# Optimization experiments

Measured on AMD Instinct MI355X. Metric: run time of the kernel, lower is better.

## Reference

```python
import jax, jax.numpy as jnp
import numpy as np

B, S, D = 4, 1024, 1024
E, F, TOPK = 16, 512, 4


def setup_inputs() -> dict:
    key = jax.random.key(0)
    k1, k2, k3, k4, k5 = jax.random.split(key, 5)
    scale = 0.02
    return {
        "x": jax.random.normal(k1, (B, S, D), dtype=jnp.float32),
        "Wr": jax.random.normal(k2, (D, E), dtype=jnp.float32) * scale,   # router
        "Wg": jax.random.normal(k3, (E, D, F), dtype=jnp.float32) * scale,  # gate proj
        "Wu": jax.random.normal(k4, (E, D, F), dtype=jnp.float32) * scale,  # up proj
        "Wd": jax.random.normal(k5, (E, F, D), dtype=jnp.float32) * scale,  # down proj
    }


def reference(x, Wr, Wg, Wu, Wd):
    b, s, d = x.shape
    xf = x.reshape(-1, d)                      # [N, D], N = B*S
    n = xf.shape[0]
    e = Wr.shape[1]

    # --- router: softmax over experts, top-k, renormalized weights ---
    probs = jax.nn.softmax(xf @ Wr, axis=-1)   # [N, E]
    w, idx = jax.lax.top_k(probs, TOPK)        # [N, K], [N, K]
    w = w / jnp.sum(w, axis=-1, keepdims=True)

    # combine weights per (token, expert); zero for unselected experts.
    # Equivalent to the per-expert where/gather/scatter-add loop in torch.
    cw = jnp.zeros((n, e), dtype=xf.dtype).at[jnp.arange(n)[:, None], idx].add(w)

    # --- per-expert gated FFN (SwiGLU), combined with routing weights ---
    def body(acc, ws):
        wg, wu, wd, c = ws                     # [D,F], [D,F], [F,D], [N]
        h = jax.nn.silu(xf @ wg) * (xf @ wu)   # [N, F]
        return acc + c[:, None] * (h @ wd), None

    out, _ = jax.lax.scan(body, jnp.zeros_like(xf), (Wg, Wu, Wd, cw.T))
    return out.reshape(b, s, d)
```

## Files before the change

### kernel.cpp

```cpp
#include <hip/hip_runtime.h>

#define N_TOK 4096
#define DIM   1024
#define NE    16
#define NF    512
#define TOPK  4
#define CAP   4096
#define NPAIR (N_TOK * TOPK)
#define MAXTILES 144
#define GU_BLOCKS (8 * MAXTILES)
#define PREPD_BLOCKS (NE * 128)

typedef _Float16 v8h __attribute__((ext_vector_type(8)));
typedef float    v4f __attribute__((ext_vector_type(4)));

__device__ __forceinline__ void prep_tile(
    const float* __restrict__ src, unsigned short* __restrict__ dst,
    int R, int C, int RIL, int e, int cbl, int rbl, float (*tile)[65])
{
    int c0 = cbl * 64, r0 = rbl * 64;
    const float* s = src + (size_t)e * R * C;
    int t = threadIdx.x;
    int tr = t >> 4, tc = (t & 15) * 4;
#pragma unroll
    for (int i = 0; i < 4; i++) {
        int row = i * 16 + tr;
        float4 v = *(const float4*)(s + (size_t)(r0 + row) * C + c0 + tc);
        tile[row][tc + 0] = v.x; tile[row][tc + 1] = v.y;
        tile[row][tc + 2] = v.z; tile[row][tc + 3] = v.w;
    }
    __syncthreads();
    int ktPerE = R >> 5;
    int cbPerE = C >> RIL;
    int imgSz  = (1 << RIL) * 32;
#pragma unroll
    for (int i = 0; i < 4; i++) {
        int nr = i * 16 + tr;
        int orow = c0 + nr;
        int k0 = r0 + tc;
        int cb = orow >> RIL;
        int r  = orow & ((1 << RIL) - 1);
        int kt = k0 >> 5;
        size_t off = ((size_t)(e * cbPerE + cb) * ktPerE + kt) * imgSz
                   + r * 32 + (k0 & 31);
        union { unsigned short u[4]; uint2 v; } p;
#pragma unroll
        for (int j = 0; j < 4; j++)
            p.u[j] = __builtin_bit_cast(unsigned short, (_Float16)tile[tc + j][nr]);
        *(uint2*)(dst + off) = p.v;
    }
}

__global__ __launch_bounds__(256) void router_prep_kernel(
    const float* __restrict__ x, const float* __restrict__ Wr,
    const float* __restrict__ Wg, const float* __restrict__ Wu,
    int* __restrict__ tokIdx, float* __restrict__ tokW,
    unsigned short* __restrict__ xb,
    unsigned short* __restrict__ Wg_t, unsigned short* __restrict__ Wu_t)
{
    __shared__ __align__(16) float tile[64][65];
    int bid = blockIdx.x;
    if (bid >= 1024) {
        int pid = bid - 1024;
        int z = pid >> 7;
        int which = z >> 4, e = z & 15;
        int bx = pid & 127;
        int cbl = bx & 7, rbl = bx >> 3;
        prep_tile(which ? Wu : Wg, which ? Wu_t : Wg_t,
                  DIM, NF, 6, e, cbl, rbl, tile);
        return;
    }
    int tid = threadIdx.x;
    int w = tid >> 6, l = tid & 63;
    int t = bid * 4 + w;

    double z[NE];
#pragma unroll
    for (int e = 0; e < NE; e++) z[e] = 0.0;
    const float* xrow = x + (size_t)t * DIM;
#pragma unroll
    for (int i = 0; i < 16; i++) {
        int d = i * 64 + l;
        double xv = (double)xrow[d];
        const float4* wr = (const float4*)(Wr + d * NE);
        float4 w0 = wr[0], w1 = wr[1], w2 = wr[2], w3 = wr[3];
        z[0]  += xv * w0.x; z[1]  += xv * w0.y; z[2]  += xv * w0.z; z[3]  += xv * w0.w;
        z[4]  += xv * w1.x; z[5]  += xv * w1.y; z[6]  += xv * w1.z; z[7]  += xv * w1.w;
        z[8]  += xv * w2.x; z[9]  += xv * w2.y; z[10] += xv * w2.z; z[11] += xv * w2.w;
        z[12] += xv * w3.x; z[13] += xv * w3.y; z[14] += xv * w3.z; z[15] += xv * w3.w;
    }
    const float4* xv4 = (const float4*)xrow;
#pragma unroll
    for (int h2 = 0; h2 < 2; h2++) {
        int base = h2 * 512 + l * 8;
        float4 a = xv4[h2 * 128 + l * 2];
        float4 b = xv4[h2 * 128 + l * 2 + 1];
        union { unsigned short u[8]; uint4 v; } p;
        p.u[0] = __builtin_bit_cast(unsigned short, (_Float16)a.x);
        p.u[1] = __builtin_bit_cast(unsigned short, (_Float16)a.y);
        p.u[2] = __builtin_bit_cast(unsigned short, (_Float16)a.z);
        p.u[3] = __builtin_bit_cast(unsigned short, (_Float16)a.w);
        p.u[4] = __builtin_bit_cast(unsigned short, (_Float16)b.x);
        p.u[5] = __builtin_bit_cast(unsigned short, (_Float16)b.y);
        p.u[6] = __builtin_bit_cast(unsigned short, (_Float16)b.z);
        p.u[7] = __builtin_bit_cast(unsigned short, (_Float16)b.w);
        *(uint4*)(xb + (size_t)t * DIM + base) = p.v;
    }
#pragma unroll
    for (int e = 0; e < NE; e++) {
#pragma unroll
        for (int m = 1; m < 64; m <<= 1) z[e] += __shfl_xor(z[e], m, 64);
    }
    if (l == 0) {
        bool taken[NE];
#pragma unroll
        for (int e = 0; e < NE; e++) taken[e] = false;
        int idx[TOPK]; double sel[TOPK];
        for (int k = 0; k < TOPK; k++) {
            int bi = 0; double bv = -1.0e300;
            for (int e = 0; e < NE; e++)
                if (!taken[e] && z[e] > bv) { bv = z[e]; bi = e; }
            taken[bi] = true; idx[k] = bi; sel[k] = bv;
        }
        double m = sel[0];
        double ex[TOPK]; double s = 0.0;
        for (int k = 0; k < TOPK; k++) { ex[k] = exp(sel[k] - m); s += ex[k]; }
        for (int k = 0; k < TOPK; k++) {
            tokIdx[t * TOPK + k] = idx[k];
            tokW[t * TOPK + k]   = (float)(ex[k] / s);
        }
    }
}

__global__ __launch_bounds__(256) void bin_kernel(
    const int* __restrict__ tokIdx,
    int* __restrict__ cnt, int* __restrict__ bpair)
{
    int e = blockIdx.x;
    int tid = threadIdx.x, lane = tid & 63, wv = tid >> 6;
    __shared__ int wsum[4];
    __shared__ int sbase;
    if (tid == 0) sbase = 0;
    __syncthreads();
    unsigned long long lt = (1ULL << lane) - 1ULL;
#pragma unroll 1
    for (int c0 = 0; c0 < NPAIR; c0 += 1024) {
        int i0 = c0 + tid * 4;
        int4 v = *(const int4*)(tokIdx + i0);
        int m[4] = {v.x == e, v.y == e, v.z == e, v.w == e};
        int r[4]; int wcnt = 0;
#pragma unroll
        for (int j = 0; j < 4; j++) {
            unsigned long long bal = __ballot(m[j] != 0);
            r[j] = wcnt + __popcll(bal & lt);
            wcnt += __popcll(bal);
        }
        if (lane == 0) wsum[wv] = wcnt;
        __syncthreads();
        int woff = sbase;
        for (int k = 0; k < wv; k++) woff += wsum[k];
#pragma unroll
        for (int j = 0; j < 4; j++)
            if (m[j]) bpair[e * CAP + woff + r[j]] = i0 + j;
        __syncthreads();
        if (tid == 0) sbase += wsum[0] + wsum[1] + wsum[2] + wsum[3];
        __syncthreads();
    }
    if (tid == 0) cnt[e] = sbase;
}

__device__ __forceinline__ int ldsw(int row, int chunk) {
    return row * 32 + (chunk ^ ((row >> 1) & 3)) * 8;
}

__device__ __forceinline__ void gload16(const unsigned short* g, unsigned short* l) {
    __builtin_amdgcn_global_load_lds(
        (const __attribute__((address_space(1))) void*)g,
        (__attribute__((address_space(3))) void*)l, 16, 0, 0);
}

__device__ __forceinline__ bool find_tile(const int* __restrict__ cnt,
                                          int ti, int& e, int& mt, int& tbase) {
    int rt = 0;
#pragma unroll 1
    for (int ee = 0; ee < NE; ee++) {
        int nt = (cnt[ee] + 127) >> 7;
        if (ti < rt + nt) { e = ee; mt = ti - rt; tbase = rt; return true; }
        rt += nt;
    }
    return false;
}

__global__ __launch_bounds__(256) void ffn_gate_up_kernel(
    const unsigned short* __restrict__ xb,
    const unsigned short* __restrict__ Wg_t,
    const unsigned short* __restrict__ Wu_t,
    const int* __restrict__ cnt,
    const int* __restrict__ bpair,
    unsigned short* __restrict__ h_t,
    const float* __restrict__ Wd,
    unsigned short* __restrict__ Wd_t)
{
    __shared__ __align__(16) unsigned char smem[33536];
    unsigned short* sX = (unsigned short*)smem;
    unsigned short* sG = (unsigned short*)(smem + 16384);
    unsigned short* sU = (unsigned short*)(smem + 24576);
    int* sTok = (int*)(smem + 32768);
    float (*tile)[65] = (float (*)[65])smem;

    int bid = blockIdx.x;
    if (bid >= GU_BLOCKS) {
        int pid = bid - GU_BLOCKS;
        int e = pid >> 7;
        int bx = pid & 127;
        int cbl = bx & 15, rbl = bx >> 4;
        prep_tile(Wd, Wd_t, NF, DIM, 7, e, cbl, rbl, tile);
        return;
    }
    int fb = bid & 7, ti = bid >> 3;
    int e, mt, tbase;
    if (!find_tile(cnt, ti, e, mt, tbase)) return;
    int count = cnt[e];

    int tid = threadIdx.x, lane = tid & 63, w = tid >> 6;
    if (tid < 128) {
        int pos = mt * 128 + tid;
        sTok[tid] = bpair[e * CAP + min(pos, count - 1)] >> 2;
    }
    __syncthreads();

    int srow0 = w * 16 + (lane >> 2);
    int srow1 = srow0 + 64;
    int spos  = lane & 3;
    int cx0 = spos ^ ((srow0 >> 1) & 3);
    int cx1 = spos ^ ((srow1 >> 1) & 3);
    const unsigned short* gX0 = xb + (size_t)sTok[srow0] * DIM + cx0 * 8;
    const unsigned short* gX1 = xb + (size_t)sTok[srow1] * DIM + cx1 * 8;
    const unsigned short* gG  = Wg_t + ((size_t)(e * 8 + fb) * 32) * 2048 + srow0 * 32 + cx0 * 8;
    const unsigned short* gU  = Wu_t + ((size_t)(e * 8 + fb) * 32) * 2048 + srow0 * 32 + cx0 * 8;
    unsigned short* dX0 = sX + (size_t)(w * 16) * 32;
    unsigned short* dX1 = sX + (size_t)(64 + w * 16) * 32;
    unsigned short* dG  = sG + (size_t)(w * 16) * 32;
    unsigned short* dU  = sU + (size_t)(w * 16) * 32;

    int row = lane & 15, q = lane >> 4;
    int rw = w & 1, cw = w >> 1;
    int aoff[4], goff[2];
#pragma unroll
    for (int mi = 0; mi < 4; mi++) aoff[mi] = ldsw(rw * 64 + mi * 16 + row, q);
#pragma unroll
    for (int ni = 0; ni < 2; ni++) goff[ni] = ldsw(cw * 32 + ni * 16 + row, q);

    v4f accG[4][2], accU[4][2];
    v4f zero = {0.f, 0.f, 0.f, 0.f};
#pragma unroll
    for (int mi = 0; mi < 4; mi++)
#pragma unroll
        for (int ni = 0; ni < 2; ni++) { accG[mi][ni] = zero; accU[mi][ni] = zero; }

#define STAGE_GU(b, kt) do {                                   \
        gload16(gX0 + (kt) * 32, dX0 + (b) * 4096);            \
        gload16(gX1 + (kt) * 32, dX1 + (b) * 4096);            \
        gload16(gG + (size_t)(kt) * 2048, dG + (b) * 2048);    \
        gload16(gU + (size_t)(kt) * 2048, dU + (b) * 2048);    \
    } while (0)

    STAGE_GU(0, 0);
    __syncthreads();

#pragma unroll 1
    for (int kt = 0; kt < 32; kt++) {
        int buf = kt & 1;
        if (kt < 31) STAGE_GU(buf ^ 1, kt + 1);
        const unsigned short* bX = sX + buf * 4096;
        const unsigned short* bGp = sG + buf * 2048;
        const unsigned short* bUp = sU + buf * 2048;
        v8h a[4], bg[2], bu[2];
#pragma unroll
        for (int mi = 0; mi < 4; mi++) a[mi] = *(const v8h*)&bX[aoff[mi]];
#pragma unroll
        for (int ni = 0; ni < 2; ni++) {
            bg[ni] = *(const v8h*)&bGp[goff[ni]];
            bu[ni] = *(const v8h*)&bUp[goff[ni]];
        }
#pragma unroll
        for (int mi = 0; mi < 4; mi++)
#pragma unroll
            for (int ni = 0; ni < 2; ni++) {
                accG[mi][ni] = __builtin_amdgcn_mfma_f32_16x16x32_f16(a[mi], bg[ni], accG[mi][ni], 0, 0, 0);
                accU[mi][ni] = __builtin_amdgcn_mfma_f32_16x16x32_f16(a[mi], bu[ni], accU[mi][ni], 0, 0, 0);
            }
        __syncthreads();
    }
#undef STAGE_GU

    size_t himg = (size_t)(tbase + mt) * 16;
#pragma unroll
    for (int mi = 0; mi < 4; mi++)
#pragma unroll
        for (int ni = 0; ni < 2; ni++) {
            int f = fb * 64 + cw * 32 + ni * 16 + row;
#pragma unroll
            for (int i = 0; i < 4; i++) {
                int rl = rw * 64 + mi * 16 + q * 4 + i;
                int pos = mt * 128 + rl;
                if (pos < count) {
                    float gv = accG[mi][ni][i];
                    float uv = accU[mi][ni][i];
                    float hv = gv * uv / (1.0f + __expf(-gv));
                    size_t off = (himg + (f >> 5)) * 4096 + rl * 32 + (f & 31);
                    h_t[off] = __builtin_bit_cast(unsigned short, (_Float16)hv);
                }
            }
        }
}

__global__ __launch_bounds__(256) void ffn_down_kernel(
    const unsigned short* __restrict__ h_t,
    const unsigned short* __restrict__ Wd_t,
    const int* __restrict__ cnt,
    const int* __restrict__ bpair,
    unsigned short* __restrict__ part)
{
    int ti = blockIdx.x, db = blockIdx.y;
    int e, mt, tbase;
    if (!find_tile(cnt, ti, e, mt, tbase)) return;
    int count = cnt[e];

    __shared__ __align__(16) unsigned short sH[2 * 128 * 32];
    __shared__ __align__(16) unsigned short sW[2 * 128 * 32];
    __shared__ int sPair[128];

    int tid = threadIdx.x, lane = tid & 63, w = tid >> 6;
    if (tid < 128) {
        int pos = mt * 128 + tid;
        sPair[tid] = bpair[e * CAP + min(pos, count - 1)];
    }
    __syncthreads();

    int srow0 = w * 16 + (lane >> 2);
    int srow1 = srow0 + 64;
    int spos  = lane & 3;
    int c0 = spos ^ ((srow0 >> 1) & 3);
    int c1 = spos ^ ((srow1 >> 1) & 3);
    const unsigned short* hbase = h_t + ((size_t)(tbase + mt) * 16) * 4096;
    const unsigned short* wbase = Wd_t + ((size_t)(e * 8 + db) * 16) * 4096;
    const unsigned short* gH0 = hbase + srow0 * 32 + c0 * 8;
    const unsigned short* gH1 = hbase + srow1 * 32 + c1 * 8;
    const unsigned short* gW0 = wbase + srow0 * 32 + c0 * 8;
    const unsigned short* gW1 = wbase + srow1 * 32 + c1 * 8;
    unsigned short* dH0 = sH + (size_t)(w * 16) * 32;
    unsigned short* dH1 = sH + (size_t)(64 + w * 16) * 32;
    unsigned short* dW0 = sW + (size_t)(w * 16) * 32;
    unsigned short* dW1 = sW + (size_t)(64 + w * 16) * 32;

    int row = lane & 15, q = lane >> 4;
    int rw = w & 1, cw = w >> 1;
    int aoff[4], boff[4];
#pragma unroll
    for (int mi = 0; mi < 4; mi++) aoff[mi] = ldsw(rw * 64 + mi * 16 + row, q);
#pragma unroll
    for (int ni = 0; ni < 4; ni++) boff[ni] = ldsw(cw * 64 + ni * 16 + row, q);

    v4f acc[4][4];
    v4f zero = {0.f, 0.f, 0.f, 0.f};
#pragma unroll
    for (int mi = 0; mi < 4; mi++)
#pragma unroll
        for (int ni = 0; ni < 4; ni++) acc[mi][ni] = zero;

#define STAGE_D(b, kt) do {                                         \
        gload16(gH0 + (size_t)(kt) * 4096, dH0 + (b) * 4096);       \
        gload16(gH1 + (size_t)(kt) * 4096, dH1 + (b) * 4096);       \
        gload16(gW0 + (size_t)(kt) * 4096, dW0 + (b) * 4096);       \
        gload16(gW1 + (size_t)(kt) * 4096, dW1 + (b) * 4096);       \
    } while (0)

    STAGE_D(0, 0);
    __syncthreads();

#pragma unroll 1
    for (int kt = 0; kt < 16; kt++) {
        int buf = kt & 1;
        if (kt < 15) STAGE_D(buf ^ 1, kt + 1);
        const unsigned short* bH = sH + buf * 4096;
        const unsigned short* bW = sW + buf * 4096;
        v8h a[4], b[4];
#pragma unroll
        for (int mi = 0; mi < 4; mi++) a[mi] = *(const v8h*)&bH[aoff[mi]];
#pragma unroll
        for (int ni = 0; ni < 4; ni++) b[ni] = *(const v8h*)&bW[boff[ni]];
#pragma unroll
        for (int mi = 0; mi < 4; mi++)
#pragma unroll
            for (int ni = 0; ni < 4; ni++)
                acc[mi][ni] = __builtin_amdgcn_mfma_f32_16x16x32_f16(a[mi], b[ni], acc[mi][ni], 0, 0, 0);
        __syncthreads();
    }
#undef STAGE_D

#pragma unroll
    for (int mi = 0; mi < 4; mi++)
#pragma unroll
        for (int ni = 0; ni < 4; ni++) {
            int col = db * 128 + cw * 64 + ni * 16 + row;
#pragma unroll
            for (int i = 0; i < 4; i++) {
                int rl = rw * 64 + mi * 16 + q * 4 + i;
                int pos = mt * 128 + rl;
                if (pos < count) {
                    int p = sPair[rl];
                    part[(size_t)p * DIM + col] =
                        __builtin_bit_cast(unsigned short, (_Float16)acc[mi][ni][i]);
                }
            }
        }
}

__global__ __launch_bounds__(256) void combine_kernel(
    const unsigned short* __restrict__ part, const float* __restrict__ tokW,
    float* __restrict__ out)
{
    int gid = blockIdx.x * 256 + threadIdx.x;
    int t = gid >> 8;
    int c = (gid & 255) * 4;
    float4 r = {0.f, 0.f, 0.f, 0.f};
#pragma unroll
    for (int k = 0; k < TOPK; k++) {
        float wk = tokW[t * TOPK + k];
        union { uint2 u; _Float16 h[4]; } cv;
        cv.u = *(const uint2*)(part + ((size_t)(t * TOPK + k)) * DIM + c);
        r.x += wk * (float)cv.h[0];
        r.y += wk * (float)cv.h[1];
        r.z += wk * (float)cv.h[2];
        r.w += wk * (float)cv.h[3];
    }
    *(float4*)(out + (size_t)t * DIM + c) = r;
}

extern "C" void kernel_launch(void* const* d_in, const int* in_sizes, int n_in,
                              void* d_out, int out_size, void* d_ws, size_t ws_size,
                              hipStream_t stream)
{
    const float* x  = (const float*)d_in[0];
    const float* Wr = (const float*)d_in[1];
    const float* Wg = (const float*)d_in[2];
    const float* Wu = (const float*)d_in[3];
    const float* Wd = (const float*)d_in[4];
    float* out = (float*)d_out;
    char* ws = (char*)d_ws;

    size_t off = 0;
    int* tokIdx = (int*)(ws + off);   off += (size_t)NPAIR * 4;
    float* tokW = (float*)(ws + off); off += (size_t)NPAIR * 4;
    int* cnt    = (int*)(ws + off);   off += 256;
    int* bpair  = (int*)(ws + off);   off += (size_t)NE * CAP * 4;
    unsigned short* xb   = (unsigned short*)(ws + off); off += (size_t)N_TOK * DIM * 2;
    unsigned short* Wg_t = (unsigned short*)(ws + off); off += (size_t)NE * DIM * NF * 2;
    unsigned short* Wu_t = (unsigned short*)(ws + off); off += (size_t)NE * DIM * NF * 2;
    unsigned short* Wd_t = (unsigned short*)(ws + off); off += (size_t)NE * DIM * NF * 2;
    unsigned short* h_t  = (unsigned short*)(ws + off); off += (size_t)MAXTILES * 16 * 4096 * 2;
    unsigned short* part = (unsigned short*)(ws + off); off += (size_t)NPAIR * DIM * 2;

    router_prep_kernel<<<1024 + 4096, 256, 0, stream>>>(
        x, Wr, Wg, Wu, tokIdx, tokW, xb, Wg_t, Wu_t);
    bin_kernel<<<NE, 256, 0, stream>>>(tokIdx, cnt, bpair);
    ffn_gate_up_kernel<<<GU_BLOCKS + PREPD_BLOCKS, 256, 0, stream>>>(
        xb, Wg_t, Wu_t, cnt, bpair, h_t, Wd, Wd_t);
    ffn_down_kernel<<<dim3(MAXTILES, 8), 256, 0, stream>>>(
        h_t, Wd_t, cnt, bpair, part);
    combine_kernel<<<(N_TOK * DIM) / (256 * 4), 256, 0, stream>>>(part, tokW, out);
}
```

Before: 271.4 us.

## Fuse combine into down-proj via atomics and relax GEMM loop barriers

Removes the separate combine kernel and the fp16 partial buffer. The down-projection now scales each result by its routing weight and atomically adds it into the output, which is zeroed by extra blocks in the router kernel. Separately, both GEMM main loops replace __syncthreads with explicit vmcnt waits and raw s_barrier so the next stage's global loads stay in flight while the current tile is consumed. The cost is fp32 atomic contention (four adds per output element) and a nondeterministic summation order.

Result: slower. 300.2 us (+10.6%).

```diff
diff --git a/kernel.cpp b/kernel.cpp
--- a/kernel.cpp
+++ b/kernel.cpp
@@ -10,6 +10,9 @@
 #define MAXTILES 144
 #define GU_BLOCKS (8 * MAXTILES)
 #define PREPD_BLOCKS (NE * 128)
+#define RP_ROUTER 1024
+#define RP_PREP   4096
+#define RP_ZERO   256
 
 typedef _Float16 v8h __attribute__((ext_vector_type(8)));
 typedef float    v4f __attribute__((ext_vector_type(4)));
@@ -56,12 +59,21 @@
     const float* __restrict__ Wg, const float* __restrict__ Wu,
     int* __restrict__ tokIdx, float* __restrict__ tokW,
     unsigned short* __restrict__ xb,
-    unsigned short* __restrict__ Wg_t, unsigned short* __restrict__ Wu_t)
+    unsigned short* __restrict__ Wg_t, unsigned short* __restrict__ Wu_t,
+    float* __restrict__ out)
 {
     __shared__ __align__(16) float tile[64][65];
     int bid = blockIdx.x;
-    if (bid >= 1024) {
-        int pid = bid - 1024;
+    if (bid >= RP_ROUTER + RP_PREP) {
+        int zb = bid - (RP_ROUTER + RP_PREP);
+        float4 z4 = {0.f, 0.f, 0.f, 0.f};
+        float4* o4 = (float4*)out + (size_t)zb * 4096 + threadIdx.x;
+#pragma unroll
+        for (int i = 0; i < 16; i++) o4[i * 256] = z4;
+        return;
+    }
+    if (bid >= RP_ROUTER) {
+        int pid = bid - RP_ROUTER;
         int z = pid >> 7;
         int which = z >> 4, e = z & 15;
         int bx = pid & 127;
@@ -266,12 +278,18 @@
     } while (0)
 
     STAGE_GU(0, 0);
-    __syncthreads();
 
 #pragma unroll 1
     for (int kt = 0; kt < 32; kt++) {
         int buf = kt & 1;
-        if (kt < 31) STAGE_GU(buf ^ 1, kt + 1);
+        if (kt < 31) {
+            STAGE_GU(buf ^ 1, kt + 1);
+            asm volatile("s_waitcnt vmcnt(4)" ::: "memory");
+        } else {
+            asm volatile("s_waitcnt vmcnt(0)" ::: "memory");
+        }
+        __builtin_amdgcn_s_barrier();
+        __builtin_amdgcn_sched_barrier(0);
         const unsigned short* bX = sX + buf * 4096;
         const unsigned short* bGp = sG + buf * 2048;
         const unsigned short* bUp = sU + buf * 2048;
@@ -290,7 +308,9 @@
                 accG[mi][ni] = __builtin_amdgcn_mfma_f32_16x16x32_f16(a[mi], bg[ni], accG[mi][ni], 0, 0, 0);
                 accU[mi][ni] = __builtin_amdgcn_mfma_f32_16x16x32_f16(a[mi], bu[ni], accU[mi][ni], 0, 0, 0);
             }
-        __syncthreads();
+        __builtin_amdgcn_sched_barrier(0);
+        __builtin_amdgcn_s_barrier();
+        __builtin_amdgcn_sched_barrier(0);
     }
 #undef STAGE_GU
 
@@ -320,7 +340,8 @@
     const unsigned short* __restrict__ Wd_t,
     const int* __restrict__ cnt,
     const int* __restrict__ bpair,
-    unsigned short* __restrict__ part)
+    const float* __restrict__ tokW,
+    float* __restrict__ out)
 {
     int ti = blockIdx.x, db = blockIdx.y;
     int e, mt, tbase;
@@ -377,12 +398,18 @@
     } while (0)
 
     STAGE_D(0, 0);
-    __syncthreads();
 
 #pragma unroll 1
     for (int kt = 0; kt < 16; kt++) {
         int buf = kt & 1;
-        if (kt < 15) STAGE_D(buf ^ 1, kt + 1);
+        if (kt < 15) {
+            STAGE_D(buf ^ 1, kt + 1);
+            asm volatile("s_waitcnt vmcnt(4)" ::: "memory");
+        } else {
+            asm volatile("s_waitcnt vmcnt(0)" ::: "memory");
+        }
+        __builtin_amdgcn_s_barrier();
+        __builtin_amdgcn_sched_barrier(0);
         const unsigned short* bH = sH + buf * 4096;
         const unsigned short* bW = sW + buf * 4096;
         v8h a[4], b[4];
@@ -395,47 +422,29 @@
 #pragma unroll
             for (int ni = 0; ni < 4; ni++)
                 acc[mi][ni] = __builtin_amdgcn_mfma_f32_16x16x32_f16(a[mi], b[ni], acc[mi][ni], 0, 0, 0);
-        __syncthreads();
+        __builtin_amdgcn_sched_barrier(0);
+        __builtin_amdgcn_s_barrier();
+        __builtin_amdgcn_sched_barrier(0);
     }
 #undef STAGE_D
 
 #pragma unroll
     for (int mi = 0; mi < 4; mi++)
 #pragma unroll
-        for (int ni = 0; ni < 4; ni++) {
-            int col = db * 128 + cw * 64 + ni * 16 + row;
-#pragma unroll
-            for (int i = 0; i < 4; i++) {
-                int rl = rw * 64 + mi * 16 + q * 4 + i;
-                int pos = mt * 128 + rl;
-                if (pos < count) {
-                    int p = sPair[rl];
-                    part[(size_t)p * DIM + col] =
-                        __builtin_bit_cast(unsigned short, (_Float16)acc[mi][ni][i]);
+        for (int i = 0; i < 4; i++) {
+            int rl = rw * 64 + mi * 16 + q * 4 + i;
+            int pos = mt * 128 + rl;
+            if (pos < count) {
+                int p = sPair[rl];
+                float wk = tokW[p];
+                float* orow = out + (size_t)(p >> 2) * DIM;
+#pragma unroll
+                for (int ni = 0; ni < 4; ni++) {
+                    int col = db * 128 + cw * 64 + ni * 16 + row;
+                    atomicAdd(orow + col, wk * acc[mi][ni][i]);
                 }
             }
         }
-}
-
-__global__ __launch_bounds__(256) void combine_kernel(
-    const unsigned short* __restrict__ part, const float* __restrict__ tokW,
-    float* __restrict__ out)
-{
-    int gid = blockIdx.x * 256 + threadIdx.x;
-    int t = gid >> 8;
-    int c = (gid & 255) * 4;
-    float4 r = {0.f, 0.f, 0.f, 0.f};
-#pragma unroll
-    for (int k = 0; k < TOPK; k++) {
-        float wk = tokW[t * TOPK + k];
-        union { uint2 u; _Float16 h[4]; } cv;
-        cv.u = *(const uint2*)(part + ((size_t)(t * TOPK + k)) * DIM + c);
-        r.x += wk * (float)cv.h[0];
-        r.y += wk * (float)cv.h[1];
-        r.z += wk * (float)cv.h[2];
-        r.w += wk * (float)cv.h[3];
-    }
-    *(float4*)(out + (size_t)t * DIM + c) = r;
 }
 
 extern "C" void kernel_launch(void* const* d_in, const int* in_sizes, int n_in,
@@ -460,14 +469,12 @@
     unsigned short* Wu_t = (unsigned short*)(ws + off); off += (size_t)NE * DIM * NF * 2;
     unsigned short* Wd_t = (unsigned short*)(ws + off); off += (size_t)NE * DIM * NF * 2;
     unsigned short* h_t  = (unsigned short*)(ws + off); off += (size_t)MAXTILES * 16 * 4096 * 2;
-    unsigned short* part = (unsigned short*)(ws + off); off += (size_t)NPAIR * DIM * 2;
-
-    router_prep_kernel<<<1024 + 4096, 256, 0, stream>>>(
-        x, Wr, Wg, Wu, tokIdx, tokW, xb, Wg_t, Wu_t);
+
+    router_prep_kernel<<<RP_ROUTER + RP_PREP + RP_ZERO, 256, 0, stream>>>(
+        x, Wr, Wg, Wu, tokIdx, tokW, xb, Wg_t, Wu_t, out);
     bin_kernel<<<NE, 256, 0, stream>>>(tokIdx, cnt, bpair);
     ffn_gate_up_kernel<<<GU_BLOCKS + PREPD_BLOCKS, 256, 0, stream>>>(
         xb, Wg_t, Wu_t, cnt, bpair, h_t, Wd, Wd_t);
     ffn_down_kernel<<<dim3(MAXTILES, 8), 256, 0, stream>>>(
-        h_t, Wd_t, cnt, bpair, part);
-    combine_kernel<<<(N_TOK * DIM) / (256 * 4), 256, 0, stream>>>(part, tokW, out);
-}
+        h_t, Wd_t, cnt, bpair, tokW, out);
+}
```

## Widen FFN tiles to 512-thread blocks with explicit vmcnt-based double buffering

Applied to the files above, without the earlier changes.

The gate/up and down GEMM kernels now run with 512 threads (8 waves) per block. Each block covers twice as many output columns: 128 F columns for gate/up and 256 D columns for down. This halves the number of blocks that re-stage the same token rows and cuts redundant loads of the gathered activation tile. The loop also replaces __syncthreads with an explicit s_waitcnt vmcnt(3) plus s_barrier, so the next stage's async global-to-LDS loads stay in flight while the current buffer is consumed. The costs are more LDS per block, fewer blocks to fill the GPU, and a Wd prep path adapted to 512 threads.

Result: no change. 275.7 us (+1.6%).

```diff
diff --git a/kernel.cpp b/kernel.cpp
--- a/kernel.cpp
+++ b/kernel.cpp
@@ -8,13 +8,16 @@
 #define CAP   4096
 #define NPAIR (N_TOK * TOPK)
 #define MAXTILES 144
-#define GU_BLOCKS (8 * MAXTILES)
+#define GU_BLOCKS (4 * MAXTILES)
+#define DN_BLOCKS (4 * MAXTILES)
 #define PREPD_BLOCKS (NE * 128)
+#define RP_ROUTER 1024
+#define RP_PREP   4096
 
 typedef _Float16 v8h __attribute__((ext_vector_type(8)));
 typedef float    v4f __attribute__((ext_vector_type(4)));
 
-__device__ __forceinline__ void prep_tile(
+__device__ __forceinline__ void prep_tile256(
     const float* __restrict__ src, unsigned short* __restrict__ dst,
     int R, int C, int RIL, int e, int cbl, int rbl, float (*tile)[65])
 {
@@ -51,6 +54,44 @@
     }
 }
 
+__device__ __forceinline__ void prep_tile512(
+    const float* __restrict__ src, unsigned short* __restrict__ dst,
+    int R, int C, int RIL, int e, int cbl, int rbl, float (*tile)[65])
+{
+    int c0 = cbl * 64, r0 = rbl * 64;
+    const float* s = src + (size_t)e * R * C;
+    int t = threadIdx.x;
+    int tr = t >> 4;
+    int tc = (t & 15) * 4;
+#pragma unroll
+    for (int i = 0; i < 2; i++) {
+        int row = i * 32 + tr;
+        float4 v = *(const float4*)(s + (size_t)(r0 + row) * C + c0 + tc);
+        tile[row][tc + 0] = v.x; tile[row][tc + 1] = v.y;
+        tile[row][tc + 2] = v.z; tile[row][tc + 3] = v.w;
+    }
+    __syncthreads();
+    int ktPerE = R >> 5;
+    int cbPerE = C >> RIL;
+    int imgSz  = (1 << RIL) * 32;
+#pragma unroll
+    for (int i = 0; i < 2; i++) {
+        int nr = i * 32 + tr;
+        int orow = c0 + nr;
+        int k0 = r0 + tc;
+        int cb = orow >> RIL;
+        int r  = orow & ((1 << RIL) - 1);
+        int kt = k0 >> 5;
+        size_t off = ((size_t)(e * cbPerE + cb) * ktPerE + kt) * imgSz
+                   + r * 32 + (k0 & 31);
+        union { unsigned short u[4]; uint2 v; } p;
+#pragma unroll
+        for (int j = 0; j < 4; j++)
+            p.u[j] = __builtin_bit_cast(unsigned short, (_Float16)tile[tc + j][nr]);
+        *(uint2*)(dst + off) = p.v;
+    }
+}
+
 __global__ __launch_bounds__(256) void router_prep_kernel(
     const float* __restrict__ x, const float* __restrict__ Wr,
     const float* __restrict__ Wg, const float* __restrict__ Wu,
@@ -60,14 +101,14 @@
 {
     __shared__ __align__(16) float tile[64][65];
     int bid = blockIdx.x;
-    if (bid >= 1024) {
-        int pid = bid - 1024;
+    if (bid >= RP_ROUTER) {
+        int pid = bid - RP_ROUTER;
         int z = pid >> 7;
         int which = z >> 4, e = z & 15;
         int bx = pid & 127;
         int cbl = bx & 7, rbl = bx >> 3;
-        prep_tile(which ? Wu : Wg, which ? Wu_t : Wg_t,
-                  DIM, NF, 6, e, cbl, rbl, tile);
+        prep_tile256(which ? Wu : Wg, which ? Wu_t : Wg_t,
+                     DIM, NF, 6, e, cbl, rbl, tile);
         return;
     }
     int tid = threadIdx.x;
@@ -191,7 +232,7 @@
     return false;
 }
 
-__global__ __launch_bounds__(256) void ffn_gate_up_kernel(
+__global__ __launch_bounds__(512, 4) void ffn_gate_up_kernel(
     const unsigned short* __restrict__ xb,
     const unsigned short* __restrict__ Wg_t,
     const unsigned short* __restrict__ Wu_t,
@@ -201,11 +242,11 @@
     const float* __restrict__ Wd,
     unsigned short* __restrict__ Wd_t)
 {
-    __shared__ __align__(16) unsigned char smem[33536];
+    __shared__ __align__(16) unsigned char smem[49664];
     unsigned short* sX = (unsigned short*)smem;
     unsigned short* sG = (unsigned short*)(smem + 16384);
-    unsigned short* sU = (unsigned short*)(smem + 24576);
-    int* sTok = (int*)(smem + 32768);
+    unsigned short* sU = (unsigned short*)(smem + 32768);
+    int* sTok = (int*)(smem + 49152);
     float (*tile)[65] = (float (*)[65])smem;
 
     int bid = blockIdx.x;
@@ -214,10 +255,10 @@
         int e = pid >> 7;
         int bx = pid & 127;
         int cbl = bx & 15, rbl = bx >> 4;
-        prep_tile(Wd, Wd_t, NF, DIM, 7, e, cbl, rbl, tile);
+        prep_tile512(Wd, Wd_t, NF, DIM, 7, e, cbl, rbl, tile);
         return;
     }
-    int fb = bid & 7, ti = bid >> 3;
+    int fb = bid & 3, ti = bid >> 2;
     int e, mt, tbase;
     if (!find_tile(cnt, ti, e, mt, tbase)) return;
     int count = cnt[e];
@@ -229,19 +270,19 @@
     }
     __syncthreads();
 
-    int srow0 = w * 16 + (lane >> 2);
-    int srow1 = srow0 + 64;
-    int spos  = lane & 3;
-    int cx0 = spos ^ ((srow0 >> 1) & 3);
-    int cx1 = spos ^ ((srow1 >> 1) & 3);
-    const unsigned short* gX0 = xb + (size_t)sTok[srow0] * DIM + cx0 * 8;
-    const unsigned short* gX1 = xb + (size_t)sTok[srow1] * DIM + cx1 * 8;
-    const unsigned short* gG  = Wg_t + ((size_t)(e * 8 + fb) * 32) * 2048 + srow0 * 32 + cx0 * 8;
-    const unsigned short* gU  = Wu_t + ((size_t)(e * 8 + fb) * 32) * 2048 + srow0 * 32 + cx0 * 8;
-    unsigned short* dX0 = sX + (size_t)(w * 16) * 32;
-    unsigned short* dX1 = sX + (size_t)(64 + w * 16) * 32;
-    unsigned short* dG  = sG + (size_t)(w * 16) * 32;
-    unsigned short* dU  = sU + (size_t)(w * 16) * 32;
+    int srow = tid >> 2;
+    int spos = tid & 3;
+    int cx = spos ^ ((srow >> 1) & 3);
+    const unsigned short* gX = xb + (size_t)sTok[srow] * DIM + cx * 8;
+    const unsigned short* gG = Wg_t
+        + ((size_t)(e * 8 + fb * 2 + (srow >> 6)) * 32) * 2048
+        + (srow & 63) * 32 + cx * 8;
+    const unsigned short* gU = Wu_t
+        + ((size_t)(e * 8 + fb * 2 + (srow >> 6)) * 32) * 2048
+        + (srow & 63) * 32 + cx * 8;
+    unsigned short* dX = sX + w * 512;
+    unsigned short* dG = sG + w * 512;
+    unsigned short* dU = sU + w * 512;
 
     int row = lane & 15, q = lane >> 4;
     int rw = w & 1, cw = w >> 1;
@@ -259,22 +300,27 @@
         for (int ni = 0; ni < 2; ni++) { accG[mi][ni] = zero; accU[mi][ni] = zero; }
 
 #define STAGE_GU(b, kt) do {                                   \
-        gload16(gX0 + (kt) * 32, dX0 + (b) * 4096);            \
-        gload16(gX1 + (kt) * 32, dX1 + (b) * 4096);            \
-        gload16(gG + (size_t)(kt) * 2048, dG + (b) * 2048);    \
-        gload16(gU + (size_t)(kt) * 2048, dU + (b) * 2048);    \
+        gload16(gX + (kt) * 32, dX + (b) * 4096);              \
+        gload16(gG + (size_t)(kt) * 2048, dG + (b) * 4096);    \
+        gload16(gU + (size_t)(kt) * 2048, dU + (b) * 4096);    \
     } while (0)
 
     STAGE_GU(0, 0);
-    __syncthreads();
 
 #pragma unroll 1
     for (int kt = 0; kt < 32; kt++) {
         int buf = kt & 1;
-        if (kt < 31) STAGE_GU(buf ^ 1, kt + 1);
+        if (kt < 31) {
+            STAGE_GU(buf ^ 1, kt + 1);
+            asm volatile("s_waitcnt vmcnt(3)" ::: "memory");
+        } else {
+            asm volatile("s_waitcnt vmcnt(0)" ::: "memory");
+        }
+        __builtin_amdgcn_s_barrier();
+        __builtin_amdgcn_sched_barrier(0);
         const unsigned short* bX = sX + buf * 4096;
-        const unsigned short* bGp = sG + buf * 2048;
-        const unsigned short* bUp = sU + buf * 2048;
+        const unsigned short* bGp = sG + buf * 4096;
+        const unsigned short* bUp = sU + buf * 4096;
         v8h a[4], bg[2], bu[2];
 #pragma unroll
         for (int mi = 0; mi < 4; mi++) a[mi] = *(const v8h*)&bX[aoff[mi]];
@@ -290,7 +336,9 @@
                 accG[mi][ni] = __builtin_amdgcn_mfma_f32_16x16x32_f16(a[mi], bg[ni], accG[mi][ni], 0, 0, 0);
                 accU[mi][ni] = __builtin_amdgcn_mfma_f32_16x16x32_f16(a[mi], bu[ni], accU[mi][ni], 0, 0, 0);
             }
-        __syncthreads();
+        __builtin_amdgcn_sched_barrier(0);
+        __builtin_amdgcn_s_barrier();
+        __builtin_amdgcn_sched_barrier(0);
     }
 #undef STAGE_GU
 
@@ -299,7 +347,7 @@
     for (int mi = 0; mi < 4; mi++)
 #pragma unroll
         for (int ni = 0; ni < 2; ni++) {
-            int f = fb * 64 + cw * 32 + ni * 16 + row;
+            int f = fb * 128 + cw * 32 + ni * 16 + row;
 #pragma unroll
             for (int i = 0; i < 4; i++) {
                 int rl = rw * 64 + mi * 16 + q * 4 + i;
@@ -315,21 +363,22 @@
         }
 }
 
-__global__ __launch_bounds__(256) void ffn_down_kernel(
+__global__ __launch_bounds__(512, 4) void ffn_down_kernel(
     const unsigned short* __restrict__ h_t,
     const unsigned short* __restrict__ Wd_t,
     const int* __restrict__ cnt,
     const int* __restrict__ bpair,
     unsigned short* __restrict__ part)
 {
-    int ti = blockIdx.x, db = blockIdx.y;
+    __shared__ __align__(16) unsigned short sH[2 * 128 * 32];
+    __shared__ __align__(16) unsigned short sW[2 * 256 * 32];
+    __shared__ int sPair[128];
+
+    int bid = blockIdx.x;
+    int db = bid & 3, ti = bid >> 2;
     int e, mt, tbase;
     if (!find_tile(cnt, ti, e, mt, tbase)) return;
     int count = cnt[e];
-
-    __shared__ __align__(16) unsigned short sH[2 * 128 * 32];
-    __shared__ __align__(16) unsigned short sW[2 * 128 * 32];
-    __shared__ int sPair[128];
 
     int tid = threadIdx.x, lane = tid & 63, w = tid >> 6;
     if (tid < 128) {
@@ -338,21 +387,18 @@
     }
     __syncthreads();
 
-    int srow0 = w * 16 + (lane >> 2);
-    int srow1 = srow0 + 64;
-    int spos  = lane & 3;
-    int c0 = spos ^ ((srow0 >> 1) & 3);
-    int c1 = spos ^ ((srow1 >> 1) & 3);
-    const unsigned short* hbase = h_t + ((size_t)(tbase + mt) * 16) * 4096;
-    const unsigned short* wbase = Wd_t + ((size_t)(e * 8 + db) * 16) * 4096;
-    const unsigned short* gH0 = hbase + srow0 * 32 + c0 * 8;
-    const unsigned short* gH1 = hbase + srow1 * 32 + c1 * 8;
-    const unsigned short* gW0 = wbase + srow0 * 32 + c0 * 8;
-    const unsigned short* gW1 = wbase + srow1 * 32 + c1 * 8;
-    unsigned short* dH0 = sH + (size_t)(w * 16) * 32;
-    unsigned short* dH1 = sH + (size_t)(64 + w * 16) * 32;
-    unsigned short* dW0 = sW + (size_t)(w * 16) * 32;
-    unsigned short* dW1 = sW + (size_t)(64 + w * 16) * 32;
+    int srow = tid >> 2;
+    int spos = tid & 3;
+    int cx = spos ^ ((srow >> 1) & 3);
+    const unsigned short* gH = h_t + ((size_t)(tbase + mt) * 16) * 4096
+                             + srow * 32 + cx * 8;
+    const unsigned short* gW0 = Wd_t + ((size_t)(e * 8 + db * 2 + 0) * 16) * 4096
+                              + srow * 32 + cx * 8;
+    const unsigned short* gW1 = Wd_t + ((size_t)(e * 8 + db * 2 + 1) * 16) * 4096
+                              + srow * 32 + cx * 8;
+    unsigned short* dH  = sH + w * 512;
+    unsigned short* dW0 = sW + w * 512;
+    unsigned short* dW1 = sW + 4096 + w * 512;
 
     int row = lane & 15, q = lane >> 4;
     int rw = w & 1, cw = w >> 1;
@@ -370,21 +416,26 @@
         for (int ni = 0; ni < 4; ni++) acc[mi][ni] = zero;
 
 #define STAGE_D(b, kt) do {                                         \
-        gload16(gH0 + (size_t)(kt) * 4096, dH0 + (b) * 4096);       \
-        gload16(gH1 + (size_t)(kt) * 4096, dH1 + (b) * 4096);       \
-        gload16(gW0 + (size_t)(kt) * 4096, dW0 + (b) * 4096);       \
-        gload16(gW1 + (size_t)(kt) * 4096, dW1 + (b) * 4096);       \
+        gload16(gH + (size_t)(kt) * 4096, dH + (b) * 4096);         \
+        gload16(gW0 + (size_t)(kt) * 4096, dW0 + (b) * 8192);       \
+        gload16(gW1 + (size_t)(kt) * 4096, dW1 + (b) * 8192);       \
     } while (0)
 
     STAGE_D(0, 0);
-    __syncthreads();
 
 #pragma unroll 1
     for (int kt = 0; kt < 16; kt++) {
         int buf = kt & 1;
-        if (kt < 15) STAGE_D(buf ^ 1, kt + 1);
+        if (kt < 15) {
+            STAGE_D(buf ^ 1, kt + 1);
+            asm volatile("s_waitcnt vmcnt(3)" ::: "memory");
+        } else {
+            asm volatile("s_waitcnt vmcnt(0)" ::: "memory");
+        }
+        __builtin_amdgcn_s_barrier();
+        __builtin_amdgcn_sched_barrier(0);
         const unsigned short* bH = sH + buf * 4096;
-        const unsigned short* bW = sW + buf * 4096;
+        const unsigned short* bW = sW + buf * 8192;
         v8h a[4], b[4];
 #pragma unroll
         for (int mi = 0; mi < 4; mi++) a[mi] = *(const v8h*)&bH[aoff[mi]];
@@ -395,7 +446,9 @@
 #pragma unroll
             for (int ni = 0; ni < 4; ni++)
                 acc[mi][ni] = __builtin_amdgcn_mfma_f32_16x16x32_f16(a[mi], b[ni], acc[mi][ni], 0, 0, 0);
-        __syncthreads();
+        __builtin_amdgcn_sched_barrier(0);
+        __builtin_amdgcn_s_barrier();
+        __builtin_amdgcn_sched_barrier(0);
     }
 #undef STAGE_D
 
@@ -403,7 +456,7 @@
     for (int mi = 0; mi < 4; mi++)
 #pragma unroll
         for (int ni = 0; ni < 4; ni++) {
-            int col = db * 128 + cw * 64 + ni * 16 + row;
+            int col = db * 256 + cw * 64 + ni * 16 + row;
 #pragma unroll
             for (int i = 0; i < 4; i++) {
                 int rl = rw * 64 + mi * 16 + q * 4 + i;
@@ -462,12 +515,12 @@
     unsigned short* h_t  = (unsigned short*)(ws + off); off += (size_t)MAXTILES * 16 * 4096 * 2;
     unsigned short* part = (unsigned short*)(ws + off); off += (size_t)NPAIR * DIM * 2;
 
-    router_prep_kernel<<<1024 + 4096, 256, 0, stream>>>(
+    router_prep_kernel<<<RP_ROUTER + RP_PREP, 256, 0, stream>>>(
         x, Wr, Wg, Wu, tokIdx, tokW, xb, Wg_t, Wu_t);
     bin_kernel<<<NE, 256, 0, stream>>>(tokIdx, cnt, bpair);
-    ffn_gate_up_kernel<<<GU_BLOCKS + PREPD_BLOCKS, 256, 0, stream>>>(
+    ffn_gate_up_kernel<<<GU_BLOCKS + PREPD_BLOCKS, 512, 0, stream>>>(
         xb, Wg_t, Wu_t, cnt, bpair, h_t, Wd, Wd_t);
-    ffn_down_kernel<<<dim3(MAXTILES, 8), 256, 0, stream>>>(
+    ffn_down_kernel<<<DN_BLOCKS, 512, 0, stream>>>(
         h_t, Wd_t, cnt, bpair, part);
     combine_kernel<<<(N_TOK * DIM) / (256 * 4), 256, 0, stream>>>(part, tokW, out);
 }
```

## Fuse expert binning into router via atomics and move Wd prep earlier

Applied to the files above, without the earlier changes.

Removes the separate bin_kernel and its tokIdx buffer. The router now appends each (token, expert) pair to per-expert lists with atomicAdd, after a memset of the counters. The Wd transpose/convert blocks move from the gate-up kernel into the router/prep kernel, so the gate-up launch only has GEMM blocks and a 2D grid. This saves one launch and the binning pass, but pair order within each expert becomes nondeterministic and the single first kernel gets larger.

Result: slower. 437.4 us (+61.1%).

```diff
diff --git a/kernel.cpp b/kernel.cpp
--- a/kernel.cpp
+++ b/kernel.cpp
@@ -8,13 +8,14 @@
 #define CAP   4096
 #define NPAIR (N_TOK * TOPK)
 #define MAXTILES 144
-#define GU_BLOCKS (8 * MAXTILES)
-#define PREPD_BLOCKS (NE * 128)
+#define RP_ROUTER 1024
+#define RP_PREP_GU 4096
+#define RP_PREP_D  2048
 
 typedef _Float16 v8h __attribute__((ext_vector_type(8)));
 typedef float    v4f __attribute__((ext_vector_type(4)));
 
-__device__ __forceinline__ void prep_tile(
+__device__ __forceinline__ void prep_tile256(
     const float* __restrict__ src, unsigned short* __restrict__ dst,
     int R, int C, int RIL, int e, int cbl, int rbl, float (*tile)[65])
 {
@@ -54,20 +55,31 @@
 __global__ __launch_bounds__(256) void router_prep_kernel(
     const float* __restrict__ x, const float* __restrict__ Wr,
     const float* __restrict__ Wg, const float* __restrict__ Wu,
-    int* __restrict__ tokIdx, float* __restrict__ tokW,
+    const float* __restrict__ Wd,
+    float* __restrict__ tokW,
     unsigned short* __restrict__ xb,
-    unsigned short* __restrict__ Wg_t, unsigned short* __restrict__ Wu_t)
+    unsigned short* __restrict__ Wg_t, unsigned short* __restrict__ Wu_t,
+    unsigned short* __restrict__ Wd_t,
+    int* __restrict__ cnt, int* __restrict__ bpair)
 {
     __shared__ __align__(16) float tile[64][65];
     int bid = blockIdx.x;
-    if (bid >= 1024) {
-        int pid = bid - 1024;
+    if (bid >= RP_ROUTER + RP_PREP_GU) {
+        int pid = bid - (RP_ROUTER + RP_PREP_GU);
+        int e = pid >> 7;
+        int bx = pid & 127;
+        int cbl = bx & 15, rbl = bx >> 4;
+        prep_tile256(Wd, Wd_t, NF, DIM, 7, e, cbl, rbl, tile);
+        return;
+    }
+    if (bid >= RP_ROUTER) {
+        int pid = bid - RP_ROUTER;
         int z = pid >> 7;
         int which = z >> 4, e = z & 15;
         int bx = pid & 127;
         int cbl = bx & 7, rbl = bx >> 3;
-        prep_tile(which ? Wu : Wg, which ? Wu_t : Wg_t,
-                  DIM, NF, 6, e, cbl, rbl, tile);
+        prep_tile256(which ? Wu : Wg, which ? Wu_t : Wg_t,
+                     DIM, NF, 6, e, cbl, rbl, tile);
         return;
     }
     int tid = threadIdx.x;
@@ -126,47 +138,12 @@
         double ex[TOPK]; double s = 0.0;
         for (int k = 0; k < TOPK; k++) { ex[k] = exp(sel[k] - m); s += ex[k]; }
         for (int k = 0; k < TOPK; k++) {
-            tokIdx[t * TOPK + k] = idx[k];
-            tokW[t * TOPK + k]   = (float)(ex[k] / s);
+            tokW[t * TOPK + k] = (float)(ex[k] / s);
+            int e = idx[k];
+            int slot = atomicAdd(&cnt[e], 1);
+            bpair[e * CAP + slot] = t * TOPK + k;
         }
     }
-}
-
-__global__ __launch_bounds__(256) void bin_kernel(
-    const int* __restrict__ tokIdx,
-    int* __restrict__ cnt, int* __restrict__ bpair)
-{
-    int e = blockIdx.x;
-    int tid = threadIdx.x, lane = tid & 63, wv = tid >> 6;
-    __shared__ int wsum[4];
-    __shared__ int sbase;
-    if (tid == 0) sbase = 0;
-    __syncthreads();
-    unsigned long long lt = (1ULL << lane) - 1ULL;
-#pragma unroll 1
-    for (int c0 = 0; c0 < NPAIR; c0 += 1024) {
-        int i0 = c0 + tid * 4;
-        int4 v = *(const int4*)(tokIdx + i0);
-        int m[4] = {v.x == e, v.y == e, v.z == e, v.w == e};
-        int r[4]; int wcnt = 0;
-#pragma unroll
-        for (int j = 0; j < 4; j++) {
-            unsigned long long bal = __ballot(m[j] != 0);
-            r[j] = wcnt + __popcll(bal & lt);
-            wcnt += __popcll(bal);
-        }
-        if (lane == 0) wsum[wv] = wcnt;
-        __syncthreads();
-        int woff = sbase;
-        for (int k = 0; k < wv; k++) woff += wsum[k];
-#pragma unroll
-        for (int j = 0; j < 4; j++)
-            if (m[j]) bpair[e * CAP + woff + r[j]] = i0 + j;
-        __syncthreads();
-        if (tid == 0) sbase += wsum[0] + wsum[1] + wsum[2] + wsum[3];
-        __syncthreads();
-    }
-    if (tid == 0) cnt[e] = sbase;
 }
 
 __device__ __forceinline__ int ldsw(int row, int chunk) {
@@ -197,27 +174,14 @@
     const unsigned short* __restrict__ Wu_t,
     const int* __restrict__ cnt,
     const int* __restrict__ bpair,
-    unsigned short* __restrict__ h_t,
-    const float* __restrict__ Wd,
-    unsigned short* __restrict__ Wd_t)
-{
-    __shared__ __align__(16) unsigned char smem[33536];
-    unsigned short* sX = (unsigned short*)smem;
-    unsigned short* sG = (unsigned short*)(smem + 16384);
-    unsigned short* sU = (unsigned short*)(smem + 24576);
-    int* sTok = (int*)(smem + 32768);
-    float (*tile)[65] = (float (*)[65])smem;
-
-    int bid = blockIdx.x;
-    if (bid >= GU_BLOCKS) {
-        int pid = bid - GU_BLOCKS;
-        int e = pid >> 7;
-        int bx = pid & 127;
-        int cbl = bx & 15, rbl = bx >> 4;
-        prep_tile(Wd, Wd_t, NF, DIM, 7, e, cbl, rbl, tile);
-        return;
-    }
-    int fb = bid & 7, ti = bid >> 3;
+    unsigned short* __restrict__ h_t)
+{
+    __shared__ __align__(16) unsigned short sX[2 * 128 * 32];
+    __shared__ __align__(16) unsigned short sG[2 * 64 * 32];
+    __shared__ __align__(16) unsigned short sU[2 * 64 * 32];
+    __shared__ int sTok[128];
+
+    int fb = blockIdx.x, ti = blockIdx.y;
     int e, mt, tbase;
     if (!find_tile(cnt, ti, e, mt, tbase)) return;
     int count = cnt[e];
@@ -451,7 +415,6 @@
     char* ws = (char*)d_ws;
 
     size_t off = 0;
-    int* tokIdx = (int*)(ws + off);   off += (size_t)NPAIR * 4;
     float* tokW = (float*)(ws + off); off += (size_t)NPAIR * 4;
     int* cnt    = (int*)(ws + off);   off += 256;
     int* bpair  = (int*)(ws + off);   off += (size_t)NE * CAP * 4;
@@ -462,11 +425,12 @@
     unsigned short* h_t  = (unsigned short*)(ws + off); off += (size_t)MAXTILES * 16 * 4096 * 2;
     unsigned short* part = (unsigned short*)(ws + off); off += (size_t)NPAIR * DIM * 2;
 
-    router_prep_kernel<<<1024 + 4096, 256, 0, stream>>>(
-        x, Wr, Wg, Wu, tokIdx, tokW, xb, Wg_t, Wu_t);
-    bin_kernel<<<NE, 256, 0, stream>>>(tokIdx, cnt, bpair);
-    ffn_gate_up_kernel<<<GU_BLOCKS + PREPD_BLOCKS, 256, 0, stream>>>(
-        xb, Wg_t, Wu_t, cnt, bpair, h_t, Wd, Wd_t);
+    hipMemsetAsync(cnt, 0, 256, stream);
+
+    router_prep_kernel<<<RP_ROUTER + RP_PREP_GU + RP_PREP_D, 256, 0, stream>>>(
+        x, Wr, Wg, Wu, Wd, tokW, xb, Wg_t, Wu_t, Wd_t, cnt, bpair);
+    ffn_gate_up_kernel<<<dim3(8, MAXTILES), 256, 0, stream>>>(
+        xb, Wg_t, Wu_t, cnt, bpair, h_t);
     ffn_down_kernel<<<dim3(MAXTILES, 8), 256, 0, stream>>>(
         h_t, Wd_t, cnt, bpair, part);
     combine_kernel<<<(N_TOK * DIM) / (256 * 4), 256, 0, stream>>>(part, tokW, out);
```
